# Kernel optimization log

Hardware: AMD Instinct MI355X
Metric: run time of the kernel (lower is better)

The kernel has to match this reference:

```python
import jax, jax.numpy as jnp
import numpy as np

N_NODES = 100000
N_EDGES = 1600000
B = 256
H = 512
HEADS = 8
DH = H // HEADS


def setup_inputs() -> dict:
    key = jax.random.key(0)
    ks = list(jax.random.split(key, 24))
    def nrm(i, shape, s=0.02):
        return jax.random.normal(ks[i], shape, jnp.float32) * s
    inp = {}
    inp["text_features"] = jax.random.normal(ks[0], (B, 768), jnp.float32)
    inp["video_features"] = jax.random.normal(ks[1], (B, 512), jnp.float32)
    inp["x"] = jax.random.normal(ks[2], (N_NODES, 64), jnp.float32)
    inp["edge_index"] = jax.random.randint(ks[3], (2, N_EDGES), 0, N_NODES, dtype=jnp.int32)
    # sorted node->graph assignment covering all B graphs (no empty segments)
    inp["batch_idx"] = ((jnp.arange(N_NODES) * B) // N_NODES).astype(jnp.int32)
    inp["Wt"] = nrm(4, (768, H)); inp["bt"] = jnp.zeros((H,), jnp.float32)
    inp["Wv"] = nrm(5, (512, H)); inp["bv"] = jnp.zeros((H,), jnp.float32)
    inp["Wq"] = nrm(6, (H, H)); inp["bq"] = jnp.zeros((H,), jnp.float32)
    inp["Wk"] = nrm(7, (H, H)); inp["bk"] = jnp.zeros((H,), jnp.float32)
    inp["Wva"] = nrm(8, (H, H)); inp["bva"] = jnp.zeros((H,), jnp.float32)
    inp["Wo"] = nrm(9, (H, H)); inp["bo"] = jnp.zeros((H,), jnp.float32)
    inp["Wf"] = nrm(10, (2 * H, H)); inp["bf"] = jnp.zeros((H,), jnp.float32)
    inp["G1W"] = nrm(11, (64, 128)); inp["G1b"] = jnp.zeros((128,), jnp.float32)
    inp["G2W"] = nrm(12, (128, 128)); inp["G2b"] = jnp.zeros((128,), jnp.float32)
    inp["G3W"] = nrm(13, (128, 256)); inp["G3b"] = jnp.zeros((256,), jnp.float32)
    inp["Wff"] = nrm(14, (H + 256, H)); inp["bff"] = jnp.zeros((H,), jnp.float32)
    inp["Wb"] = nrm(15, (H, 2)); inp["bb"] = jnp.zeros((2,), jnp.float32)
    inp["Wa"] = nrm(16, (H, 2)); inp["ba"] = jnp.zeros((2,), jnp.float32)
    return inp


def _gcn_conv(h, W, b, src, dst, dis):
    # PyG GCNConv: linear transform, symmetric-normalized aggregation w/ self-loops, bias
    hw = h @ W                                       # [N, C]
    norm = dis[src] * dis[dst]                       # [E]
    msg = hw[src] * norm[:, None]                    # [E, C]
    agg = jax.ops.segment_sum(msg, dst, num_segments=h.shape[0])
    agg = agg + hw * (dis * dis)[:, None]            # self-loop messages
    return agg + b


def reference(text_features, video_features, x, edge_index, batch_idx, Wt, bt, Wv, bv, Wq, bq, Wk, bk, Wva, bva, Wo, bo, Wf, bf, G1W, G1b, G2W, G2b, G3W, G3b, Wff, bff, Wb, bb, Wa, ba):
    # encoders (dropout is eval-mode no-op)
    text_enc = jax.nn.relu(text_features @ Wt + bt)      # [B, H]
    video_enc = jax.nn.relu(video_features @ Wv + bv)    # [B, H]
    # multihead attention; torch seq lens are both 1 (batch acts as N)
    q = (text_enc @ Wq + bq).reshape(B, HEADS, 1, DH)
    k = (video_enc @ Wk + bk).reshape(B, HEADS, 1, DH)
    v = (video_enc @ Wva + bva).reshape(B, HEADS, 1, DH)
    scores = jnp.einsum('bhqd,bhkd->bhqk', q, k) / np.float32(np.sqrt(DH))
    w = jax.nn.softmax(scores, axis=-1)
    attn = jnp.einsum('bhqk,bhkd->bhqd', w, v).reshape(B, H)
    text_attended = attn @ Wo + bo
    # multimodal fusion
    fused = jax.nn.relu(jnp.concatenate([text_attended, video_enc], axis=1) @ Wf + bf)
    # GCN stack
    src, dst = edge_index[0], edge_index[1]
    deg = jax.ops.segment_sum(jnp.ones((N_EDGES,), jnp.float32), dst, num_segments=N_NODES) + 1.0
    dis = jax.lax.rsqrt(deg)
    h = jax.nn.elu(_gcn_conv(x, G1W, G1b, src, dst, dis))
    h = jax.nn.elu(_gcn_conv(h, G2W, G2b, src, dst, dis))
    h = _gcn_conv(h, G3W, G3b, src, dst, dis)            # [N, 256]
    # per-graph mean pooling (the original per-batch Python loop, as one segment-mean)
    counts = jax.ops.segment_sum(jnp.ones((N_NODES,), jnp.float32), batch_idx, num_segments=B)
    pooled = jax.ops.segment_sum(h, batch_idx, num_segments=B) / counts[:, None]  # [B, 256]
    # final fusion + classifier heads
    final = jax.nn.relu(jnp.concatenate([fused, pooled], axis=1) @ Wff + bff)
    bullying = jax.nn.log_softmax(final @ Wb + bb, axis=1)
    aggression = jax.nn.log_softmax(final @ Wa + ba, axis=1)
    return bullying, aggression
```

## Files before the change

kernel.cpp:

```cpp
#include <hip/hip_runtime.h>
#include <hip/hip_bf16.h>
#include <hip/hip_fp8.h>

#define N_NODES 100000
#define NPAD    100096
#define N_EDGES 1600000
#define BATCH   256
#define HDIM    512

typedef unsigned short u16;
typedef unsigned char  u8;
typedef __attribute__((ext_vector_type(8))) short bf16x8;
typedef __attribute__((ext_vector_type(8))) unsigned short u16x8;
typedef __attribute__((ext_vector_type(8))) unsigned char u8x8;
typedef __attribute__((ext_vector_type(4))) float f32x4;

__device__ __forceinline__ float bf2f(u16 u) {
    union { unsigned i; float f; } v; v.i = ((unsigned)u) << 16; return v.f;
}
__device__ __forceinline__ u16 f2bf(float f) {
    __hip_bfloat16 h = __float2bfloat16(f);
    return *reinterpret_cast<u16*>(&h);
}
__device__ __forceinline__ u8 f2fp8(float f) {
    __hip_fp8_e4m3 q(f); return (u8)q.__x;
}
__device__ __forceinline__ float fp82f(u8 b) {
    __hip_fp8_e4m3 q; q.__x = (__hip_fp8_storage_t)b; return (float)q;
}

template<int K, int ACT, int SCALE, int F8>
__global__ __launch_bounds__(256) void gemm_mfma(
        const u16* __restrict__ A, const u16* __restrict__ Wt,
        const float* __restrict__ bias, const float* __restrict__ dis,
        void* __restrict__ Cv, int N) {
    constexpr int RB = K * 2;
    __shared__ u16 As[128 * K];
    __shared__ u16 Bs[128 * K];
    const int tid  = threadIdx.x;
    const int lane = tid & 63;
    const int w    = tid >> 6;
    const int wr   = w >> 1, wc = w & 1;
    const int row0 = blockIdx.y * 128;
    const int col0 = blockIdx.x * 128;

    constexpr int WB     = 128 * RB / 4;
    constexpr int PASSES = WB / 1024;
    const size_t Abase = (size_t)row0 * K;
    const size_t Bbase = (size_t)col0 * K;
    #pragma unroll
    for (int p = 0; p < PASSES; ++p) {
        int Lb  = w * WB + p * 1024;
        int L   = Lb + lane * 16;
        int row = L / RB;
        int cb  = L % RB;
        int scb = cb ^ ((row & 7) << 4);
        const u16* ga = A  + Abase + (size_t)row * K + (scb >> 1);
        const u16* gb = Wt + Bbase + (size_t)row * K + (scb >> 1);
        __builtin_amdgcn_global_load_lds((const __attribute__((address_space(1))) void*)ga,
            (__attribute__((address_space(3))) void*)&As[Lb >> 1], 16, 0, 0);
        __builtin_amdgcn_global_load_lds((const __attribute__((address_space(1))) void*)gb,
            (__attribute__((address_space(3))) void*)&Bs[Lb >> 1], 16, 0, 0);
    }
    asm volatile("s_waitcnt vmcnt(0)" ::: "memory");
    __syncthreads();

    const int rl = lane & 15;
    const int kg = lane >> 4;
    f32x4 acc[4][4] = {};
    #pragma unroll
    for (int s = 0; s < K / 32; ++s) {
        bf16x8 af[4], bg[4];
        #pragma unroll
        for (int m = 0; m < 4; ++m) {
            int row = wr * 64 + m * 16 + rl;
            int cb  = s * 64 + kg * 16;
            int scb = cb ^ ((row & 7) << 4);
            af[m] = *(const bf16x8*)&As[(row * RB + scb) >> 1];
        }
        #pragma unroll
        for (int n = 0; n < 4; ++n) {
            int row = wc * 64 + n * 16 + rl;
            int cb  = s * 64 + kg * 16;
            int scb = cb ^ ((row & 7) << 4);
            bg[n] = *(const bf16x8*)&Bs[(row * RB + scb) >> 1];
        }
        #pragma unroll
        for (int m = 0; m < 4; ++m)
            #pragma unroll
            for (int n = 0; n < 4; ++n)
                acc[m][n] = __builtin_amdgcn_mfma_f32_16x16x32_bf16(af[m], bg[n], acc[m][n], 0, 0, 0);
    }

    #pragma unroll
    for (int m = 0; m < 4; ++m) {
        #pragma unroll
        for (int r = 0; r < 4; ++r) {
            int grow = row0 + wr * 64 + m * 16 + kg * 4 + r;
            float ds = SCALE ? dis[grow] : 1.f;
            #pragma unroll
            for (int n = 0; n < 4; ++n) {
                int gcol = col0 + wc * 64 + n * 16 + rl;
                float v = acc[m][n][r] + bias[gcol];
                if (ACT == 2) v = v > 0.f ? v : expm1f(v);
                v *= ds;
                if (F8) ((u8*)Cv)[(size_t)grow * N + gcol] = f2fp8(v);
                else    ((u16*)Cv)[(size_t)grow * N + gcol] = f2bf(v);
            }
        }
    }
}

template<int ACT>
__global__ __launch_bounds__(256) void gemm64(
        const u16* __restrict__ A, const u16* __restrict__ Wt,
        const float* __restrict__ bias, u16* __restrict__ C,
        int K, int lda, int ldc) {
    __shared__ u16 As[64 * 64];
    __shared__ u16 Bs[64 * 64];
    const int tid  = threadIdx.x;
    const int lane = tid & 63;
    const int w    = tid >> 6;
    const int wr   = w >> 1, wc = w & 1;
    const int row0 = blockIdx.y * 64;
    const int col0 = blockIdx.x * 64;
    const int rl = lane & 15;
    const int kg = lane >> 4;
    f32x4 acc[2][2] = {};

    for (int k0 = 0; k0 < K; k0 += 64) {
        #pragma unroll
        for (int p = 0; p < 2; ++p) {
            int Lb  = w * 2048 + p * 1024;
            int L   = Lb + lane * 16;
            int row = L >> 7;
            int cb  = L & 127;
            int scb = cb ^ ((row & 7) << 4);
            const u16* ga = A  + (size_t)(row0 + row) * lda + k0 + (scb >> 1);
            const u16* gb = Wt + (size_t)(col0 + row) * K   + k0 + (scb >> 1);
            __builtin_amdgcn_global_load_lds((const __attribute__((address_space(1))) void*)ga,
                (__attribute__((address_space(3))) void*)&As[Lb >> 1], 16, 0, 0);
            __builtin_amdgcn_global_load_lds((const __attribute__((address_space(1))) void*)gb,
                (__attribute__((address_space(3))) void*)&Bs[Lb >> 1], 16, 0, 0);
        }
        asm volatile("s_waitcnt vmcnt(0)" ::: "memory");
        __syncthreads();
        #pragma unroll
        for (int s = 0; s < 2; ++s) {
            bf16x8 af[2], bg[2];
            #pragma unroll
            for (int m = 0; m < 2; ++m) {
                int row = wr * 32 + m * 16 + rl;
                int cb  = s * 64 + kg * 16;
                int scb = cb ^ ((row & 7) << 4);
                af[m] = *(const bf16x8*)&As[(row * 128 + scb) >> 1];
            }
            #pragma unroll
            for (int n = 0; n < 2; ++n) {
                int row = wc * 32 + n * 16 + rl;
                int cb  = s * 64 + kg * 16;
                int scb = cb ^ ((row & 7) << 4);
                bg[n] = *(const bf16x8*)&Bs[(row * 128 + scb) >> 1];
            }
            #pragma unroll
            for (int m = 0; m < 2; ++m)
                #pragma unroll
                for (int n = 0; n < 2; ++n)
                    acc[m][n] = __builtin_amdgcn_mfma_f32_16x16x32_bf16(af[m], bg[n], acc[m][n], 0, 0, 0);
        }
        __syncthreads();
    }

    #pragma unroll
    for (int m = 0; m < 2; ++m) {
        #pragma unroll
        for (int r = 0; r < 4; ++r) {
            int grow = row0 + wr * 32 + m * 16 + kg * 4 + r;
            #pragma unroll
            for (int n = 0; n < 2; ++n) {
                int gcol = col0 + wc * 32 + n * 16 + rl;
                float v = acc[m][n][r] + bias[gcol];
                if (ACT == 1) v = fmaxf(v, 0.f);
                C[(size_t)grow * ldc + gcol] = f2bf(v);
            }
        }
    }
}

template<int K, int N>
__device__ __forceinline__ void tw(const float* __restrict__ W, u16* __restrict__ Wt, int t) {
    int n = t / K, k = t - n * K;
    Wt[t] = f2bf(W[(size_t)k * N + n]);
}

#define DEG_BLKS 6250

__global__ void prep_deg(const int* __restrict__ dstE, int* __restrict__ deg,
                         int* __restrict__ slot,
                         const float* __restrict__ G1W, u16* __restrict__ g1wt,
                         const float* __restrict__ G2W, u16* __restrict__ g2wt,
                         const float* __restrict__ Wv,  u16* __restrict__ WvT,
                         const float* __restrict__ Wva, u16* __restrict__ WvaT,
                         const float* __restrict__ Wo,  u16* __restrict__ WoT,
                         const float* __restrict__ Wf,  u16* __restrict__ WfT,
                         const float* __restrict__ video, u16* __restrict__ vidbf) {
    int bid = blockIdx.x;
    const int tid = threadIdx.x;
    if (bid < DEG_BLKS) {
        int e = bid * 256 + tid;
        slot[e] = atomicAdd(&deg[dstE[e]], 1);
        return;
    }
    bid -= DEG_BLKS;
    if (bid < 32)        { tw<64, 128>  (G1W, g1wt, bid * 256 + tid); }
    else if (bid < 96)   { tw<128, 128> (G2W, g2wt, (bid - 32) * 256 + tid); }
    else if (bid < 1120) { tw<512, 512> (Wv,  WvT,  (bid - 96) * 256 + tid); }
    else if (bid < 2144) { tw<512, 512> (Wva, WvaT, (bid - 1120) * 256 + tid); }
    else if (bid < 3168) { tw<512, 512> (Wo,  WoT,  (bid - 2144) * 256 + tid); }
    else if (bid < 5216) { tw<1024, 512>(Wf,  WfT,  (bid - 3168) * 256 + tid); }
    else { int t = (bid - 5216) * 256 + tid; vidbf[t] = f2bf(video[t]); }
}

__global__ void final_fused(const u16* __restrict__ fusedb,
                            const float* __restrict__ pooled, const float* __restrict__ counts,
                            const float* __restrict__ G3W, const float* __restrict__ G3b,
                            const float* __restrict__ Wff, const float* __restrict__ bff,
                            const float* __restrict__ Wb,  const float* __restrict__ bb,
                            const float* __restrict__ Wa,  const float* __restrict__ ba,
                            float* __restrict__ out) {
    __shared__ float cat[768], fin[512], pp[128];
    __shared__ float rd[4][4];
    const int b = blockIdx.x, tid = threadIdx.x;
    cat[tid] = bf2f(fusedb[b * 512 + tid]);
    cat[tid + 256] = bf2f(fusedb[b * 512 + 256 + tid]);
    float inv = 1.f / counts[b];
    if (tid < 128) pp[tid] = pooled[b * 128 + tid] * inv;
    __syncthreads();
    {
        float s = G3b[tid];
        #pragma unroll 8
        for (int k = 0; k < 128; ++k) s += pp[k] * G3W[k * 256 + tid];
        cat[512 + tid] = s;
    }
    __syncthreads();
    {
        float a0 = bff[tid], a1 = bff[tid + 256];
        #pragma unroll 8
        for (int k = 0; k < 768; ++k) {
            float xv = cat[k];
            a0 += xv * Wff[k * 512 + tid];
            a1 += xv * Wff[k * 512 + tid + 256];
        }
        fin[tid] = fmaxf(a0, 0.f);
        fin[tid + 256] = fmaxf(a1, 0.f);
    }
    __syncthreads();
    float z0 = 0.f, z1 = 0.f, y0 = 0.f, y1 = 0.f;
    for (int k = tid; k < 512; k += 256) {
        float f = fin[k];
        z0 += f * Wb[2 * k];
        z1 += f * Wb[2 * k + 1];
        y0 += f * Wa[2 * k];
        y1 += f * Wa[2 * k + 1];
    }
    #pragma unroll
    for (int off = 32; off > 0; off >>= 1) {
        z0 += __shfl_down(z0, off);
        z1 += __shfl_down(z1, off);
        y0 += __shfl_down(y0, off);
        y1 += __shfl_down(y1, off);
    }
    int ww = tid >> 6;
    if ((tid & 63) == 0) { rd[ww][0] = z0; rd[ww][1] = z1; rd[ww][2] = y0; rd[ww][3] = y1; }
    __syncthreads();
    if (tid == 0) {
        float Z0 = rd[0][0] + rd[1][0] + rd[2][0] + rd[3][0] + bb[0];
        float Z1 = rd[0][1] + rd[1][1] + rd[2][1] + rd[3][1] + bb[1];
        float Y0 = rd[0][2] + rd[1][2] + rd[2][2] + rd[3][2] + ba[0];
        float Y1 = rd[0][3] + rd[1][3] + rd[2][3] + rd[3][3] + ba[1];
        float m = fmaxf(Z0, Z1);
        float l = m + logf(expf(Z0 - m) + expf(Z1 - m));
        out[b * 2 + 0] = Z0 - l;
        out[b * 2 + 1] = Z1 - l;
        float m2 = fmaxf(Y0, Y1);
        float l2 = m2 + logf(expf(Y0 - m2) + expf(Y1 - m2));
        out[512 + b * 2 + 0] = Y0 - l2;
        out[512 + b * 2 + 1] = Y1 - l2;
    }
}

__global__ void scan1(const int* __restrict__ in, int* __restrict__ out,
                      int* __restrict__ bsum, float* __restrict__ dis, int n) {
    __shared__ int ts[256];
    const int tid = threadIdx.x;
    const int base = blockIdx.x * 1024;
    int v[4];
    #pragma unroll
    for (int i = 0; i < 4; ++i) {
        int idx = base + tid * 4 + i;
        v[i] = (idx < n) ? in[idx] : 0;
        if (idx < NPAD) dis[idx] = rsqrtf((float)v[i] + 1.f);
    }
    ts[tid] = v[0] + v[1] + v[2] + v[3];
    __syncthreads();
    for (int off = 1; off < 256; off <<= 1) {
        int val = (tid >= off) ? ts[tid - off] : 0;
        __syncthreads();
        ts[tid] += val;
        __syncthreads();
    }
    int run = (tid == 0) ? 0 : ts[tid - 1];
    if (tid == 255) bsum[blockIdx.x] = ts[255];
    #pragma unroll
    for (int i = 0; i < 4; ++i) {
        int idx = base + tid * 4 + i;
        if (idx < n) out[idx] = run;
        run += v[i];
    }
}

__global__ void scan2(int* __restrict__ bsum, int nb) {
    int l = threadIdx.x;
    int a = (l < nb) ? bsum[l] : 0;
    int b = (l + 64 < nb) ? bsum[l + 64] : 0;
    int oa = a, ob = b;
    #pragma unroll
    for (int off = 1; off < 64; off <<= 1) {
        int t = __shfl_up(a, off);
        if (l >= off) a += t;
    }
    int totA = __shfl(a, 63);
    #pragma unroll
    for (int off = 1; off < 64; off <<= 1) {
        int t = __shfl_up(b, off);
        if (l >= off) b += t;
    }
    if (l < nb) bsum[l] = a - oa;
    if (l + 64 < nb) bsum[l + 64] = totA + b - ob;
}

#define SCAT_BLKS 6250
#define SCALE_BLKS 25000
__global__ void scatter_scale(const int* __restrict__ srcE, const int* __restrict__ dstE,
                              const int* __restrict__ partial, const int* __restrict__ bsum,
                              const int* __restrict__ slot,
                              int2* __restrict__ csr_sd, int* __restrict__ rowptr,
                              const float* __restrict__ x, const float* __restrict__ dis,
                              u16* __restrict__ hs0) {
    const int bid = blockIdx.x, tid = threadIdx.x;
    if (bid < SCAT_BLKS) {
        int e = bid * 256 + tid;
        if (e <= N_NODES) rowptr[e] = (e < N_NODES) ? (partial[e] + bsum[e >> 10]) : N_EDGES;
        int d = dstE[e];
        csr_sd[partial[d] + bsum[d >> 10] + slot[e]] = make_int2(srcE[e], d);
        return;
    }
    int t = (bid - SCAT_BLKS) * 256 + tid;
    hs0[t] = f2bf(x[t] * dis[t >> 6]);
}

__global__ void csr_agg64(const u16* __restrict__ Hs, const int* __restrict__ rowptr,
                          const int2* __restrict__ csr_sd, const float* __restrict__ dis,
                          u16* __restrict__ out) {
    int node = blockIdx.x * 4 + (threadIdx.x >> 6);
    if (node >= N_NODES) return;
    int lane = threadIdx.x & 63;
    int g  = lane >> 3;
    int cl = lane & 7;
    int s0 = rowptr[node], s1 = rowptr[node + 1];
    float a[8] = {};
    if (g == 0) {
        u16x8 v = *(const u16x8*)&Hs[(size_t)node * 64 + cl * 8];
        #pragma unroll
        for (int j = 0; j < 8; ++j) a[j] = bf2f(v[j]);
    }
    int e = s0 + g;
    while (e + 24 < s1) {
        int sA = csr_sd[e].x, sB = csr_sd[e + 8].x;
        int sC = csr_sd[e + 16].x, sD = csr_sd[e + 24].x;
        u16x8 vA = *(const u16x8*)&Hs[(size_t)sA * 64 + cl * 8];
        u16x8 vB = *(const u16x8*)&Hs[(size_t)sB * 64 + cl * 8];
        u16x8 vC = *(const u16x8*)&Hs[(size_t)sC * 64 + cl * 8];
        u16x8 vD = *(const u16x8*)&Hs[(size_t)sD * 64 + cl * 8];
        #pragma unroll
        for (int j = 0; j < 8; ++j)
            a[j] += (bf2f(vA[j]) + bf2f(vB[j])) + (bf2f(vC[j]) + bf2f(vD[j]));
        e += 32;
    }
    while (e < s1) {
        int s = csr_sd[e].x;
        u16x8 v = *(const u16x8*)&Hs[(size_t)s * 64 + cl * 8];
        #pragma unroll
        for (int j = 0; j < 8; ++j) a[j] += bf2f(v[j]);
        e += 8;
    }
    #pragma unroll
    for (int m = 8; m < 64; m <<= 1)
        #pragma unroll
        for (int j = 0; j < 8; ++j) a[j] += __shfl_xor(a[j], m);
    if (g == 0) {
        float dd = dis[node];
        u16x8 o;
        #pragma unroll
        for (int j = 0; j < 8; ++j) o[j] = f2bf(a[j] * dd);
        *(u16x8*)&out[(size_t)node * 64 + cl * 8] = o;
    }
}

__global__ void csr_agg_fp8(const u8* __restrict__ Hs, const int* __restrict__ rowptr,
                            const int2* __restrict__ csr_sd, const float* __restrict__ dis,
                            u16* __restrict__ out) {
    int node = blockIdx.x * 4 + (threadIdx.x >> 6);
    if (node >= N_NODES) return;
    int lane = threadIdx.x & 63;
    int g  = lane >> 4;
    int cl = lane & 15;
    int s0 = rowptr[node], s1 = rowptr[node + 1];
    float a[8] = {};
    if (g == 0) {
        u8x8 v = *(const u8x8*)&Hs[(size_t)node * 128 + cl * 8];
        #pragma unroll
        for (int j = 0; j < 8; ++j) a[j] = fp82f(v[j]);
    }
    int e = s0 + g;
    while (e + 12 < s1) {
        int sA = csr_sd[e].x, sB = csr_sd[e + 4].x;
        int sC = csr_sd[e + 8].x, sD = csr_sd[e + 12].x;
        u8x8 vA = *(const u8x8*)&Hs[(size_t)sA * 128 + cl * 8];
        u8x8 vB = *(const u8x8*)&Hs[(size_t)sB * 128 + cl * 8];
        u8x8 vC = *(const u8x8*)&Hs[(size_t)sC * 128 + cl * 8];
        u8x8 vD = *(const u8x8*)&Hs[(size_t)sD * 128 + cl * 8];
        #pragma unroll
        for (int j = 0; j < 8; ++j)
            a[j] += (fp82f(vA[j]) + fp82f(vB[j])) + (fp82f(vC[j]) + fp82f(vD[j]));
        e += 16;
    }
    while (e < s1) {
        int s = csr_sd[e].x;
        u8x8 v = *(const u8x8*)&Hs[(size_t)s * 128 + cl * 8];
        #pragma unroll
        for (int j = 0; j < 8; ++j) a[j] += fp82f(v[j]);
        e += 4;
    }
    #pragma unroll
    for (int m = 16; m < 64; m <<= 1)
        #pragma unroll
        for (int j = 0; j < 8; ++j) a[j] += __shfl_xor(a[j], m);
    if (g == 0) {
        float dd = dis[node];
        u16x8 o;
        #pragma unroll
        for (int j = 0; j < 8; ++j) o[j] = f2bf(a[j] * dd);
        *(u16x8*)&out[(size_t)node * 128 + cl * 8] = o;
    }
}

#define PE_BLKS 1563
#define PS_BLKS 391
__global__ __launch_bounds__(256) void pool_fused(
        const u8* __restrict__ Hs, const int2* __restrict__ csr_sd,
        const float* __restrict__ dis, const int* __restrict__ batch,
        float* __restrict__ pooled, float* __restrict__ counts) {
    __shared__ float bins[2][128];
    __shared__ int b0s;
    const int tid = threadIdx.x;
    const int bid = blockIdx.x;
    if (tid < 128) { bins[0][tid] = 0.f; bins[1][tid] = 0.f; }
    if (bid < PE_BLKS) {
        const int base = bid * 1024;
        const int end  = min(base + 1024, N_EDGES);
        if (tid == 0) b0s = batch[csr_sd[base].y];
        __syncthreads();
        const int b0 = b0s;
        const int lane = tid & 63, w = tid >> 6;
        const int slot = w * 4 + (lane >> 4);
        const int cl = lane & 15;
        float a[8] = {};
        int bcur = b0;
        for (int e = base + slot; e < end; e += 16) {
            int2 sd = csr_sd[e];
            float dd = dis[sd.y];
            int b = batch[sd.y];
            if (b != bcur) {
                if (bcur - b0 < 2) {
                    #pragma unroll
                    for (int j = 0; j < 8; ++j) atomicAdd(&bins[bcur - b0][cl * 8 + j], a[j]);
                } else {
                    #pragma unroll
                    for (int j = 0; j < 8; ++j) atomicAdd(&pooled[bcur * 128 + cl * 8 + j], a[j]);
                }
                #pragma unroll
                for (int j = 0; j < 8; ++j) a[j] = 0.f;
                bcur = b;
            }
            u8x8 v = *(const u8x8*)&Hs[(size_t)sd.x * 128 + cl * 8];
            #pragma unroll
            for (int j = 0; j < 8; ++j) a[j] += fp82f(v[j]) * dd;
        }
        if (bcur - b0 < 2) {
            #pragma unroll
            for (int j = 0; j < 8; ++j) atomicAdd(&bins[bcur - b0][cl * 8 + j], a[j]);
        } else {
            #pragma unroll
            for (int j = 0; j < 8; ++j) atomicAdd(&pooled[bcur * 128 + cl * 8 + j], a[j]);
        }
        __syncthreads();
        int bin = tid >> 7, c = tid & 127;
        if (b0 + bin < BATCH) atomicAdd(&pooled[(b0 + bin) * 128 + c], bins[bin][c]);
    } else {
        const int base = (bid - PE_BLKS) * 256;
        const int end  = min(base + 256, N_NODES);
        if (tid == 0) b0s = batch[base];
        __syncthreads();
        const int b0 = b0s;
        const int c = tid & 127, h = tid >> 7;
        float a = 0.f; int bcur = b0; int cnt = 0;
        for (int n = base + h; n < end; n += 2) {
            int b = batch[n];
            if (b != bcur) {
                atomicAdd(&bins[bcur - b0][c], a);
                if (c == 0) atomicAdd(&counts[bcur], (float)cnt);
                a = 0.f; cnt = 0; bcur = b;
            }
            a += fp82f(Hs[(size_t)n * 128 + c]) * dis[n];
            cnt++;
        }
        atomicAdd(&bins[bcur - b0][c], a);
        if (c == 0) atomicAdd(&counts[bcur], (float)cnt);
        __syncthreads();
        int bin = tid >> 7, cc = tid & 127;
        if (b0 + bin < BATCH) atomicAdd(&pooled[(b0 + bin) * 128 + cc], bins[bin][cc]);
    }
}

extern "C" void kernel_launch(void* const* d_in, const int* in_sizes, int n_in,
                              void* d_out, int out_size, void* d_ws, size_t ws_size,
                              hipStream_t stream) {
    const float* video = (const float*)d_in[1];
    const float* x     = (const float*)d_in[2];
    const int*   eidx  = (const int*)d_in[3];
    const int*   batch = (const int*)d_in[4];
    const float* Wv  = (const float*)d_in[7],  *bv  = (const float*)d_in[8];
    const float* Wva = (const float*)d_in[13], *bva = (const float*)d_in[14];
    const float* Wo  = (const float*)d_in[15], *bo  = (const float*)d_in[16];
    const float* Wf  = (const float*)d_in[17], *bf  = (const float*)d_in[18];
    const float* G1W = (const float*)d_in[19], *G1b = (const float*)d_in[20];
    const float* G2W = (const float*)d_in[21], *G2b = (const float*)d_in[22];
    const float* G3W = (const float*)d_in[23], *G3b = (const float*)d_in[24];
    const float* Wff = (const float*)d_in[25], *bff = (const float*)d_in[26];
    const float* Wb  = (const float*)d_in[27], *bb  = (const float*)d_in[28];
    const float* Wa  = (const float*)d_in[29], *ba  = (const float*)d_in[30];
    const int* srcE = eidx;
    const int* dstE = eidx + N_EDGES;

    char* wsc = (char*)d_ws;
    size_t off = 0;
    auto alloc = [&](size_t bytes) { char* p = wsc + off; off += (bytes + 255) & ~(size_t)255; return p; };
    u16*   bufA    = (u16*)  alloc((size_t)NPAD * 128 * 2);
    u16*   bufB    = (u16*)  alloc((size_t)NPAD * 128 * 2);
    float* dis     = (float*)alloc(NPAD * 4);
    int*   deg     = (int*)  alloc(NPAD * 4);
    float* pooled  = (float*)alloc((BATCH * 128 + BATCH) * 4);
    float* counts  = pooled + BATCH * 128;
    int*   partial = (int*)  alloc(N_NODES * 4);
    int*   rowptr  = (int*)  alloc((N_NODES + 1) * 4);
    int*   slot    = (int*)  alloc((size_t)N_EDGES * 4);
    int2*  csr_sd  = (int2*) alloc((size_t)N_EDGES * 8);
    int*   bsum    = (int*)  alloc(128 * 4);
    u16*   g1wt    = (u16*)  alloc(128 * 64 * 2);
    u16*   g2wt    = (u16*)  alloc(128 * 128 * 2);
    u16*   WvT     = (u16*)  alloc(512 * 512 * 2);
    u16*   WvaT    = (u16*)  alloc(512 * 512 * 2);
    u16*   WoT     = (u16*)  alloc(512 * 512 * 2);
    u16*   WfT     = (u16*)  alloc(512 * 1024 * 2);
    u16*   vidbf   = (u16*)  alloc(BATCH * 512 * 2);
    u16*   catb    = (u16*)  alloc(BATCH * 1024 * 2);
    u16*   vattnb  = (u16*)  alloc(BATCH * 512 * 2);
    u16*   fusedb  = (u16*)  alloc(BATCH * 512 * 2);

    const int NB = (N_NODES + 1023) / 1024;

    hipMemsetAsync(deg, 0, NPAD * 4 + (BATCH * 128 + BATCH) * 4, stream);

    prep_deg<<<DEG_BLKS + 5728, 256, 0, stream>>>(dstE, deg, slot,
        G1W, g1wt, G2W, g2wt, Wv, WvT, Wva, WvaT, Wo, WoT, Wf, WfT, video, vidbf);

    scan1<<<NB, 256, 0, stream>>>(deg, partial, bsum, dis, N_NODES);
    scan2<<<1, 64, 0, stream>>>(bsum, NB);
    scatter_scale<<<SCAT_BLKS + SCALE_BLKS, 256, 0, stream>>>(
        srcE, dstE, partial, bsum, slot, csr_sd, rowptr, x, dis, bufA);

    dim3 fe512(8, 4);
    gemm64<1><<<fe512, 256, 0, stream>>>(vidbf, WvT, bv, catb + 512, 512, 512, 1024);
    gemm64<0><<<fe512, 256, 0, stream>>>(catb + 512, WvaT, bva, vattnb, 512, 1024, 512);
    gemm64<0><<<fe512, 256, 0, stream>>>(vattnb, WoT, bo, catb, 512, 512, 1024);
    gemm64<1><<<fe512, 256, 0, stream>>>(catb, WfT, bf, fusedb, 1024, 1024, 512);

    csr_agg64<<<(N_NODES + 3) / 4, 256, 0, stream>>>(bufA, rowptr, csr_sd, dis, bufB);
    gemm_mfma<64, 2, 1, 1><<<dim3(1, NPAD / 128), 256, 0, stream>>>(
        bufB, g1wt, G1b, dis, bufA, 128);
    csr_agg_fp8<<<(N_NODES + 3) / 4, 256, 0, stream>>>((const u8*)bufA, rowptr, csr_sd, dis, bufB);
    gemm_mfma<128, 2, 1, 1><<<dim3(1, NPAD / 128), 256, 0, stream>>>(
        bufB, g2wt, G2b, dis, bufA, 128);
    pool_fused<<<PE_BLKS + PS_BLKS, 256, 0, stream>>>((const u8*)bufA, csr_sd, dis,
                                                      batch, pooled, counts);

    final_fused<<<BATCH, 256, 0, stream>>>(fusedb, pooled, counts, G3W, G3b,
                                           Wff, bff, Wb, bb, Wa, ba, (float*)d_out);
}
```

Baseline: 427.5 us.

## Pack dis and batch into CSR edge records and unroll edge pooling loop

The scatter kernel now stores each edge's destination normalisation (as bf16) and graph id in the y field of the CSR edge record, replacing the raw destination index. The pooling kernel therefore no longer does two dependent gathers (dis and batch) per edge. The pooling edge loop is also restructured: it issues four edge loads and row loads at a time for more memory-level parallelism. Per-edge sums go into two register bins, with atomics only for rarer graph ids, so the segment-change branch and flushes are gone. In exchange, dis is rounded to bf16 precision, and any other kernel that reads csr_sd.y as a node index would now be wrong.

```diff
diff --git a/kernel.cpp b/kernel.cpp
--- a/kernel.cpp
+++ b/kernel.cpp
@@ -343,7 +343,7 @@
 #define SCALE_BLKS 25000
 __global__ void scatter_scale(const int* __restrict__ srcE, const int* __restrict__ dstE,
                               const int* __restrict__ partial, const int* __restrict__ bsum,
-                              const int* __restrict__ slot,
+                              const int* __restrict__ slot, const int* __restrict__ batch,
                               int2* __restrict__ csr_sd, int* __restrict__ rowptr,
                               const float* __restrict__ x, const float* __restrict__ dis,
                               u16* __restrict__ hs0) {
@@ -352,7 +352,8 @@
         int e = bid * 256 + tid;
         if (e <= N_NODES) rowptr[e] = (e < N_NODES) ? (partial[e] + bsum[e >> 10]) : N_EDGES;
         int d = dstE[e];
-        csr_sd[partial[d] + bsum[d >> 10] + slot[e]] = make_int2(srcE[e], d);
+        unsigned y = ((unsigned)f2bf(dis[d]) << 16) | (unsigned)batch[d];
+        csr_sd[partial[d] + bsum[d >> 10] + slot[e]] = make_int2(srcE[e], (int)y);
         return;
     }
     int t = (bid - SCAT_BLKS) * 256 + tid;
@@ -462,47 +463,58 @@
         const float* __restrict__ dis, const int* __restrict__ batch,
         float* __restrict__ pooled, float* __restrict__ counts) {
     __shared__ float bins[2][128];
-    __shared__ int b0s;
     const int tid = threadIdx.x;
     const int bid = blockIdx.x;
     if (tid < 128) { bins[0][tid] = 0.f; bins[1][tid] = 0.f; }
+    __syncthreads();
     if (bid < PE_BLKS) {
         const int base = bid * 1024;
         const int end  = min(base + 1024, N_EDGES);
-        if (tid == 0) b0s = batch[csr_sd[base].y];
-        __syncthreads();
-        const int b0 = b0s;
+        const int b0 = ((unsigned)csr_sd[base].y) & 0xffffu;
         const int lane = tid & 63, w = tid >> 6;
         const int slot = w * 4 + (lane >> 4);
         const int cl = lane & 15;
-        float a[8] = {};
-        int bcur = b0;
-        for (int e = base + slot; e < end; e += 16) {
+        float a0[8] = {}, a1[8] = {};
+        int e = base + slot;
+        #define ACC(sd, v)                                                     \
+            {                                                                  \
+                unsigned y = (unsigned)(sd).y;                                 \
+                int bin = (int)(y & 0xffffu) - b0;                             \
+                float dd = bf2f((u16)(y >> 16));                               \
+                if (bin == 0) {                                                \
+                    _Pragma("unroll")                                          \
+                    for (int j = 0; j < 8; ++j) a0[j] += fp82f((v)[j]) * dd;   \
+                } else if (bin == 1) {                                         \
+                    _Pragma("unroll")                                          \
+                    for (int j = 0; j < 8; ++j) a1[j] += fp82f((v)[j]) * dd;   \
+                } else {                                                       \
+                    _Pragma("unroll")                                          \
+                    for (int j = 0; j < 8; ++j)                                \
+                        atomicAdd(&pooled[(b0 + bin) * 128 + cl * 8 + j],      \
+                                  fp82f((v)[j]) * dd);                         \
+                }                                                              \
+            }
+        while (e + 48 < end) {
+            int2 sd0 = csr_sd[e],      sd1 = csr_sd[e + 16];
+            int2 sd2 = csr_sd[e + 32], sd3 = csr_sd[e + 48];
+            u8x8 v0 = *(const u8x8*)&Hs[(size_t)sd0.x * 128 + cl * 8];
+            u8x8 v1 = *(const u8x8*)&Hs[(size_t)sd1.x * 128 + cl * 8];
+            u8x8 v2 = *(const u8x8*)&Hs[(size_t)sd2.x * 128 + cl * 8];
+            u8x8 v3 = *(const u8x8*)&Hs[(size_t)sd3.x * 128 + cl * 8];
+            ACC(sd0, v0); ACC(sd1, v1); ACC(sd2, v2); ACC(sd3, v3);
+            e += 64;
+        }
+        while (e < end) {
             int2 sd = csr_sd[e];
-            float dd = dis[sd.y];
-            int b = batch[sd.y];
-            if (b != bcur) {
-                if (bcur - b0 < 2) {
-                    #pragma unroll
-                    for (int j = 0; j < 8; ++j) atomicAdd(&bins[bcur - b0][cl * 8 + j], a[j]);
-                } else {
-                    #pragma unroll
-                    for (int j = 0; j < 8; ++j) atomicAdd(&pooled[bcur * 128 + cl * 8 + j], a[j]);
-                }
-                #pragma unroll
-                for (int j = 0; j < 8; ++j) a[j] = 0.f;
-                bcur = b;
-            }
             u8x8 v = *(const u8x8*)&Hs[(size_t)sd.x * 128 + cl * 8];
-            #pragma unroll
-            for (int j = 0; j < 8; ++j) a[j] += fp82f(v[j]) * dd;
-        }
-        if (bcur - b0 < 2) {
-            #pragma unroll
-            for (int j = 0; j < 8; ++j) atomicAdd(&bins[bcur - b0][cl * 8 + j], a[j]);
-        } else {
-            #pragma unroll
-            for (int j = 0; j < 8; ++j) atomicAdd(&pooled[bcur * 128 + cl * 8 + j], a[j]);
+            ACC(sd, v);
+            e += 16;
+        }
+        #undef ACC
+        #pragma unroll
+        for (int j = 0; j < 8; ++j) {
+            atomicAdd(&bins[0][cl * 8 + j], a0[j]);
+            atomicAdd(&bins[1][cl * 8 + j], a1[j]);
         }
         __syncthreads();
         int bin = tid >> 7, c = tid & 127;
@@ -510,9 +522,7 @@
     } else {
         const int base = (bid - PE_BLKS) * 256;
         const int end  = min(base + 256, N_NODES);
-        if (tid == 0) b0s = batch[base];
-        __syncthreads();
-        const int b0 = b0s;
+        const int b0 = batch[base];
         const int c = tid & 127, h = tid >> 7;
         float a = 0.f; int bcur = b0; int cnt = 0;
         for (int n = base + h; n < end; n += 2) {
@@ -588,7 +598,7 @@
     scan1<<<NB, 256, 0, stream>>>(deg, partial, bsum, dis, N_NODES);
     scan2<<<1, 64, 0, stream>>>(bsum, NB);
     scatter_scale<<<SCAT_BLKS + SCALE_BLKS, 256, 0, stream>>>(
-        srcE, dstE, partial, bsum, slot, csr_sd, rowptr, x, dis, bufA);
+        srcE, dstE, partial, bsum, slot, batch, csr_sd, rowptr, x, dis, bufA);
 
     dim3 fe512(8, 4);
     gemm64<1><<<fe512, 256, 0, stream>>>(vidbf, WvT, bv, catb + 512, 512, 512, 1024);
```

Result: slower. 442.1 us (+3.4%).
